# Kernel tuning notes

Measured on AMD Instinct MI355X. Metric: run time of the kernel, lower is better.

The kernel has to match this reference:

```python
import jax, jax.numpy as jnp
import numpy as np
from jax import lax

H = 2048          # hidden_size
NAH = 16          # num attn heads
AHD = H // NAH    # 128
NFH = 4           # num lact (fast-weight) heads
FHD = H // NFH    # 512 = d_in = d_out
DH = FHD          # d_h = d_in * inter_multi (1.0)
WIN = 1024        # sliding window
CHUNK = 512       # lact chunk size
B, S = 2, 2048
ROPE_BASE = 500000.0
EPS = 1e-6
BASE_LR_INV = 0.001 + float(np.log(-np.expm1(-0.001)))  # inv_softplus(1e-3)


def rms_norm(x, w):
    return x * lax.rsqrt(jnp.mean(x * x, axis=-1, keepdims=True) + EPS) * w


def silu(x):
    return x * jax.nn.sigmoid(x)


def silu_backprop(dy, x):
    sg = jax.nn.sigmoid(x)
    return dy * sg * (1.0 + x * (1.0 - sg))


def apply_rope(q, k):
    # q,k: [b,s,h,d]; non-interleaved (half-split) rotary, matching flash-attn RotaryEmbedding
    d = q.shape[-1]
    inv_freq = 1.0 / (ROPE_BASE ** (jnp.arange(0, d, 2, dtype=jnp.float32) / d))
    t = jnp.arange(q.shape[1], dtype=jnp.float32)
    freqs = jnp.outer(t, inv_freq)                       # [s, d/2]
    cos = jnp.cos(freqs)[None, :, None, :]
    sin = jnp.sin(freqs)[None, :, None, :]
    def rot(x):
        x1, x2 = jnp.split(x, 2, axis=-1)
        return jnp.concatenate([x1 * cos - x2 * sin, x2 * cos + x1 * sin], axis=-1)
    return rot(q), rot(k)


def sliding_window_attn(q, k, v):
    # [b,s,h,d]; causal sliding-window attention
    s = q.shape[1]
    scale = 1.0 / np.sqrt(q.shape[-1])
    i = jnp.arange(s)[:, None]
    j = jnp.arange(s)[None, :]
    mask = (j <= i) & (i - j < WIN)                      # [s,s]
    scores = jnp.einsum('bihd,bjhd->bhij', q, k) * scale
    scores = jnp.where(mask[None, None], scores, -jnp.inf)
    p = jax.nn.softmax(scores, axis=-1)
    return jnp.einsum('bhij,bjhd->bihd', p, v)


def setup_inputs() -> dict:
    key = jax.random.key(0)
    ks = jax.random.split(key, 10)
    def n(k, shape, scale):
        return jax.random.normal(k, shape, dtype=jnp.float32) * scale
    return {
        'hidden_states': n(ks[0], (B, S, H), 1.0),
        'attn_qkv_w': n(ks[1], (3 * H, H), 0.02),
        'attn_o_w': n(ks[2], (H, H), 0.02),
        'q_norm_w': jnp.ones((H,), jnp.float32),
        'k_norm_w': jnp.ones((H,), jnp.float32),
        'mlp_norm_w': jnp.ones((H,), jnp.float32),
        'mlp_qkv_w': n(ks[3], (3 * NFH * FHD, H), 0.02),
        'mlp_o_w': n(ks[4], (H, NFH * FHD), 0.02),
        'lr_w': n(ks[5], (3 * NFH, H), 0.02),
        'lr_b': jnp.zeros((3 * NFH,), jnp.float32),
        'w0': n(ks[6], (NFH, DH, FHD), 1.0 / np.sqrt(FHD)),
        'w1': n(ks[7], (NFH, FHD, DH), 1.0 / np.sqrt(DH)),
        'w2': n(ks[8], (NFH, DH, FHD), 1.0 / np.sqrt(FHD)),
        'ttt_norm_w': jnp.ones((FHD,), jnp.float32),
    }


def _forward(hidden_states, attn_qkv_w, attn_o_w, q_norm_w, k_norm_w, mlp_norm_w,
             mlp_qkv_w, mlp_o_w, lr_w, lr_b, w0, w1, w2, ttt_norm_w):
    b, s, _ = hidden_states.shape
    # ---- sliding window attention (token mixer) ----
    qkv = hidden_states @ attn_qkv_w.T
    q, k, v = jnp.split(qkv, 3, axis=-1)
    q = rms_norm(q, q_norm_w)
    k = rms_norm(k, k_norm_w)
    q = q.reshape(b, s, NAH, AHD)
    k = k.reshape(b, s, NAH, AHD)
    v = v.reshape(b, s, NAH, AHD)
    q, k = apply_rope(q, k)
    o = sliding_window_attn(q, k, v)
    attn_out = o.reshape(b, s, H) @ attn_o_w.T

    # ---- TTT-MLP SwiGLU fast-weight channel mixer after SWA ----
    x = rms_norm(attn_out, mlp_norm_w)
    fqkv = x @ mlp_qkv_w.T
    fq, fk, fv = jnp.split(fqkv, 3, axis=-1)
    fq, fk, fv = silu(fq), silu(fk), silu(fv)
    fq = fq.reshape(b, s, NFH, FHD)
    fk = fk.reshape(b, s, NFH, FHD)
    fv = fv.reshape(b, s, NFH, FHD)
    fq = fq / jnp.clip(jnp.linalg.norm(fq, axis=-1, keepdims=True), 1e-6)
    fk = fk / jnp.clip(jnp.linalg.norm(fk, axis=-1, keepdims=True), 1e-6)

    # per-token lrs (mamba parameterization: softplus(proj + inv_softplus(base_lr)))
    lr = jax.nn.softplus(x @ lr_w.T + lr_b + BASE_LR_INV)   # [b,s,3*NFH]
    l0, l1, l2 = jnp.split(lr, 3, axis=-1)                  # each [b,s,NFH]

    nc = s // CHUNK
    def chunkify(t):  # [b,s,h,d] -> [nc,b,h,c,d]
        return t.reshape(b, nc, CHUNK, t.shape[2], t.shape[3]).transpose(1, 0, 3, 2, 4)
    qs = chunkify(fq)
    ks_ = chunkify(fk)
    vs = chunkify(fv)
    l0s = chunkify(l0[..., None])
    l1s = chunkify(l1[..., None])
    l2s = chunkify(l2[..., None])

    w0b = jnp.broadcast_to(w0[None], (b,) + w0.shape)
    w1b = jnp.broadcast_to(w1[None], (b,) + w1.shape)
    w2b = jnp.broadcast_to(w2[None], (b,) + w2.shape)

    def step(carry, inp):
        cw0, cw1, cw2 = carry
        qc, kc, vc, lr0, lr1, lr2 = inp   # qc/kc/vc: [b,h,c,d]; lr*: [b,h,c,1]
        # apply current fast weights to queries of this chunk (apply-then-update)
        gq = jnp.einsum('bhed,bhcd->bhce', cw0, qc)
        hq = silu(gq) * jnp.einsum('bhed,bhcd->bhce', cw2, qc)
        oc = jnp.einsum('bhoe,bhce->bhco', cw1, hq)
        # update fast weights with this chunk's (k, v) under negative dot-product loss
        gk = jnp.einsum('bhed,bhcd->bhce', cw0, kc)      # gate pre-act
        hbm = jnp.einsum('bhed,bhcd->bhce', cw2, kc)     # hidden before mul
        hid = silu(gk) * hbm
        dhid = jnp.einsum('bhoe,bhco->bhce', cw1, vc)    # grad wrt hidden
        dhbm = dhid * silu(gk)
        dgate = dhid * hbm
        dgpre = silu_backprop(dgate, gk)
        nw1 = cw1 + jnp.einsum('bhco,bhce->bhoe', vc * lr1, hid)
        nw0 = cw0 + jnp.einsum('bhce,bhcd->bhed', dgpre, kc * lr0)
        nw2 = cw2 + jnp.einsum('bhce,bhcd->bhed', dhbm, kc * lr2)
        return (nw0, nw1, nw2), oc

    _, ocs = lax.scan(step, (w0b, w1b, w2b), (qs, ks_, vs, l0s, l1s, l2s))
    o_fw = ocs.transpose(1, 0, 3, 2, 4).reshape(b, s, NFH, FHD)
    o_fw = rms_norm(o_fw, ttt_norm_w)
    ttt_out = o_fw.reshape(b, s, NFH * FHD) @ mlp_o_w.T
    return attn_out + ttt_out


def reference(hidden_states, attn_qkv_w, attn_o_w, q_norm_w, k_norm_w, mlp_norm_w,
              mlp_qkv_w, mlp_o_w, lr_w, lr_b, w0, w1, w2, ttt_norm_w):
    return _forward(hidden_states, attn_qkv_w, attn_o_w, q_norm_w, k_norm_w, mlp_norm_w,
                    mlp_qkv_w, mlp_o_w, lr_w, lr_b, w0, w1, w2, ttt_norm_w)
```

## Files before the change

kernel.cpp:

```cpp
#include <hip/hip_runtime.h>
#include <cmath>

typedef unsigned short u16;
typedef unsigned int u32;
typedef short s16x8 __attribute__((ext_vector_type(8)));
typedef short s16x4 __attribute__((ext_vector_type(4)));
typedef float f32x4 __attribute__((ext_vector_type(4)));

#define DEV static __device__ __forceinline__

DEV float b2f(u16 h) { return __uint_as_float(((u32)h) << 16); }
DEV u16 f2b(float f) {
  u32 u = __float_as_uint(f);
  u = (u + 0x7FFFu + ((u >> 16) & 1u)) >> 16;
  return (u16)u;
}
DEV float siluf(float x) { return x / (1.f + __expf(-x)); }

DEV void gload16(const void* g, void* l) {
  __builtin_amdgcn_global_load_lds((const __attribute__((address_space(1))) void*)g,
                                   (__attribute__((address_space(3))) void*)l, 16, 0, 0);
}

struct GemmDesc {
  const u16* A; const u16* B;
  float* C; const float* Cin;
  u16* Cb; u16* CbT;
  long sAb, sAh, sBb, sBh, sCb_, sCh_, sCbb, sCbh, sCtb, sCth;
  int lda, ldb, ldc, ldcb, ldct, K;
};
struct GemmBatch { GemmDesc d[5]; int nbh; };

__global__ __launch_bounds__(256) void gemm_bt(GemmBatch gb) {
  int di = blockIdx.z / gb.nbh;
  int bh = blockIdx.z % gb.nbh;
  GemmDesc d = gb.d[di];
  __shared__ __align__(16) u16 As[2][4096];
  __shared__ __align__(16) u16 Bs[2][4096];
  int tid = threadIdx.x, w = tid >> 6, l = tid & 63;
  int b2 = bh >> 2, h2 = bh & 3;
  const u16* Ab = d.A + (long)b2 * d.sAb + (long)h2 * d.sAh + (long)blockIdx.y * 128 * d.lda;
  const u16* Bb = d.B + (long)b2 * d.sBb + (long)h2 * d.sBh + (long)blockIdx.x * 128 * d.ldb;
  int srow = l >> 2, scol = (l & 3) * 8;
  f32x4 acc[4][4] = {};
  int nk = d.K >> 5;

  auto stage = [&](int buf, int kt) {
    #pragma unroll
    for (int i = 0; i < 2; ++i) {
      int chunk = i * 4 + w;
      int row = chunk * 16 + srow;
      gload16(Ab + (long)row * d.lda + kt * 32 + scol, &As[buf][chunk * 512]);
      gload16(Bb + (long)row * d.ldb + kt * 32 + scol, &Bs[buf][chunk * 512]);
    }
  };

  stage(0, 0);
  asm volatile("s_waitcnt vmcnt(0)" ::: "memory");
  __syncthreads();

  int wr = (w >> 1) * 64, wc = (w & 1) * 64;
  int fro = l & 15, fko = (l >> 4) * 8;

  for (int kt = 0; kt < nk; ++kt) {
    int buf = kt & 1;
    if (kt + 1 < nk) stage(buf ^ 1, kt + 1);
    s16x8 af[4], bfr[4];
    #pragma unroll
    for (int m = 0; m < 4; ++m) af[m] = *(const s16x8*)&As[buf][(wr + m * 16 + fro) * 32 + fko];
    #pragma unroll
    for (int n = 0; n < 4; ++n) bfr[n] = *(const s16x8*)&Bs[buf][(wc + n * 16 + fro) * 32 + fko];
    #pragma unroll
    for (int m = 0; m < 4; ++m)
      #pragma unroll
      for (int n = 0; n < 4; ++n)
        acc[m][n] = __builtin_amdgcn_mfma_f32_16x16x32_bf16(af[m], bfr[n], acc[m][n], 0, 0, 0);
    asm volatile("s_waitcnt vmcnt(0)" ::: "memory");
    __syncthreads();
  }

  float* Cp = d.C ? d.C + (long)b2 * d.sCb_ + (long)h2 * d.sCh_ : nullptr;
  const float* Ci = d.Cin ? d.Cin + (long)b2 * d.sCb_ + (long)h2 * d.sCh_ : nullptr;
  u16* Cbp = d.Cb ? d.Cb + (long)b2 * d.sCbb + (long)h2 * d.sCbh : nullptr;
  u16* Ctp = d.CbT ? d.CbT + (long)b2 * d.sCtb + (long)h2 * d.sCth : nullptr;
  long rbase = (long)blockIdx.y * 128 + wr + (l >> 4) * 4;
  long cbase = (long)blockIdx.x * 128 + wc + (l & 15);
  #pragma unroll
  for (int m = 0; m < 4; ++m)
    #pragma unroll
    for (int n = 0; n < 4; ++n)
      #pragma unroll
      for (int j = 0; j < 4; ++j) {
        long r = rbase + m * 16 + j;
        long c = cbase + n * 16;
        float v = acc[m][n][j];
        if (Ci) v += Ci[r * d.ldc + c];
        if (Cp) Cp[r * d.ldc + c] = v;
        if (Cbp) Cbp[r * d.ldcb + c] = f2b(v);
        if (Ctp) Ctp[c * d.ldct + r] = f2b(v);
      }
}

__global__ __launch_bounds__(256) void convk(const float* __restrict__ in, u16* __restrict__ outp) {
  long i = ((long)blockIdx.x * 256 + threadIdx.x) * 4;
  float4 v = *(const float4*)(in + i);
  u16 o[4] __attribute__((aligned(8))) = {f2b(v.x), f2b(v.y), f2b(v.z), f2b(v.w)};
  *(s16x4*)&outp[i] = *(const s16x4*)o;
}

__global__ __launch_bounds__(256) void norm_rope_kernel(const u16* __restrict__ qkv,
    const float* __restrict__ qw, const float* __restrict__ kw,
    u16* __restrict__ qg, u16* __restrict__ kg, u16* __restrict__ vg) {
  __shared__ float qsh[2048], ksh[2048];
  __shared__ float red[2][4];
  int t = blockIdx.x, tid = threadIdx.x, w = tid >> 6, l = tid & 63;
  int s = t & 2047;
  const u16* row = qkv + (long)t * 6144;
  s16x8 vq = *(const s16x8*)&row[tid * 8];
  s16x8 vk = *(const s16x8*)&row[2048 + tid * 8];
  float sq = 0.f, sk = 0.f;
  #pragma unroll
  for (int i = 0; i < 8; ++i) {
    float a = b2f((u16)vq[i]); qsh[tid * 8 + i] = a; sq += a * a;
    float c = b2f((u16)vk[i]); ksh[tid * 8 + i] = c; sk += c * c;
  }
  *(s16x8*)&vg[(long)t * 2048 + tid * 8] = *(const s16x8*)&row[4096 + tid * 8];
  #pragma unroll
  for (int mk = 32; mk; mk >>= 1) { sq += __shfl_xor(sq, mk, 64); sk += __shfl_xor(sk, mk, 64); }
  if (l == 0) { red[0][w] = sq; red[1][w] = sk; }
  __syncthreads();
  float rq = rsqrtf((red[0][0] + red[0][1] + red[0][2] + red[0][3]) * (1.f / 2048.f) + 1e-6f);
  float rk = rsqrtf((red[1][0] + red[1][1] + red[1][2] + red[1][3]) * (1.f / 2048.f) + 1e-6f);
  const float lf = 13.122363377404329f / 64.f;
  #pragma unroll
  for (int ii = 0; ii < 4; ++ii) {
    int pid = tid + 256 * ii;
    int h = pid >> 6, dpos = pid & 63;
    float invf = expf(-(float)dpos * lf);
    float ang = (float)s * invf;
    float sn, cs;
    sincosf(ang, &sn, &cs);
    int i1 = h * 128 + dpos, i2 = i1 + 64;
    float q1 = qsh[i1] * rq * qw[i1], q2 = qsh[i2] * rq * qw[i2];
    qg[(long)t * 2048 + i1] = f2b(q1 * cs - q2 * sn);
    qg[(long)t * 2048 + i2] = f2b(q2 * cs + q1 * sn);
    float k1 = ksh[i1] * rk * kw[i1], k2v = ksh[i2] * rk * kw[i2];
    kg[(long)t * 2048 + i1] = f2b(k1 * cs - k2v * sn);
    kg[(long)t * 2048 + i2] = f2b(k2v * cs + k1 * sn);
  }
}

__global__ __launch_bounds__(256) void vtrans_kernel(const u16* __restrict__ v, u16* __restrict__ vT) {
  __shared__ u16 T[64][74];
  int tid = threadIdx.x;
  int bh = blockIdx.z, b = bh >> 4, h = bh & 15;
  int ts = blockIdx.x * 64, dg = blockIdx.y * 64;
  int r = tid >> 2, c0 = (tid & 3) * 16;
  const u16* src = v + ((long)b * 2048 + ts + r) * 2048 + h * 128 + dg + c0;
  *(s16x8*)&T[r][c0] = *(const s16x8*)src;
  *(s16x8*)&T[r][c0 + 8] = *(const s16x8*)(src + 8);
  __syncthreads();
  int d = tid >> 2, tg = (tid & 3) * 16;
  u16 a[16] __attribute__((aligned(16)));
  #pragma unroll
  for (int j = 0; j < 16; ++j) a[j] = T[tg + j][d];
  u16* dst = vT + ((long)bh * 128 + dg + d) * 2048 + ts + tg;
  *(s16x8*)dst = ((const s16x8*)a)[0];
  *(s16x8*)(dst + 8) = ((const s16x8*)a)[1];
}

__global__ __launch_bounds__(256, 3) void attn_kernel(const u16* __restrict__ qg, const u16* __restrict__ kg,
                                                      const u16* __restrict__ vT, u16* __restrict__ og) {
  __shared__ __align__(16) u16 Ks[64][136];
  __shared__ __align__(16) u16 Vt[128][72];
  __shared__ __align__(16) u16 Ps[4][16][72];
  int tid = threadIdx.x, w = tid >> 6, l = tid & 63;
  int h = blockIdx.y, b = blockIdx.z;
  int qs = blockIdx.x * 64;
  long tokb = (long)b * 2048;
  int fr = l & 15, fg = l >> 4;
  int wrow = qs + w * 16;

  s16x8 qf[4];
  #pragma unroll
  for (int ks = 0; ks < 4; ++ks)
    qf[ks] = *(const s16x8*)&qg[(tokb + wrow + fr) * 2048 + h * 128 + ks * 32 + fg * 8];

  f32x4 oacc[8] = {};
  float mrun[4], lrun[4];
  #pragma unroll
  for (int j = 0; j < 4; ++j) { mrun[j] = -__builtin_inff(); lrun[j] = 0.f; }

  int lo = qs - 1023;
  int t0 = lo > 0 ? (lo >> 6) : 0;
  int t1 = (qs + 63) >> 6;
  const float scale = 0.088388347648318447f;

  const u16* kbase = kg + tokb * 2048 + h * 128;
  const u16* vbase = vT + (long)(b * 16 + h) * 128 * 2048;

  s16x8 kreg[4], vreg[4];
  auto loadrg = [&](int kvs) {
    #pragma unroll
    for (int it = 0; it < 4; ++it) {
      int idx = it * 256 + tid;
      kreg[it] = *(const s16x8*)&kbase[(long)(kvs + (idx >> 4)) * 2048 + (idx & 15) * 8];
      vreg[it] = *(const s16x8*)&vbase[(long)(idx >> 3) * 2048 + kvs + (idx & 7) * 8];
    }
  };
  auto writelds = [&]() {
    #pragma unroll
    for (int it = 0; it < 4; ++it) {
      int idx = it * 256 + tid;
      *(s16x8*)&Ks[idx >> 4][(idx & 15) * 8] = kreg[it];
      *(s16x8*)&Vt[idx >> 3][(idx & 7) * 8] = vreg[it];
    }
  };

  loadrg(t0 << 6);
  writelds();
  __syncthreads();

  for (int kt = t0; kt <= t1; ++kt) {
    int kvs = kt << 6;
    if (kt < t1) loadrg((kt + 1) << 6);
    bool active = (kvs <= wrow + 15);
    if (active) {
      f32x4 st[4] = {};
      #pragma unroll
      for (int ct = 0; ct < 4; ++ct)
        #pragma unroll
        for (int ks = 0; ks < 4; ++ks) {
          s16x8 kf = *(const s16x8*)&Ks[ct * 16 + fr][ks * 32 + fg * 8];
          st[ct] = __builtin_amdgcn_mfma_f32_16x16x32_bf16(qf[ks], kf, st[ct], 0, 0, 0);
        }
      bool needm = (kvs + 63 > wrow) || (kvs < wrow - 1008);
      float mx[4];
      #pragma unroll
      for (int j = 0; j < 4; ++j) mx[j] = -__builtin_inff();
      #pragma unroll
      for (int ct = 0; ct < 4; ++ct)
        #pragma unroll
        for (int j = 0; j < 4; ++j) {
          float s = st[ct][j] * scale;
          if (needm) {
            int r = wrow + fg * 4 + j;
            int c = kvs + ct * 16 + fr;
            if (c > r || (r - c) >= 1024) s = -__builtin_inff();
          }
          st[ct][j] = s;
          mx[j] = fmaxf(mx[j], s);
        }
      #pragma unroll
      for (int mk = 8; mk; mk >>= 1)
        #pragma unroll
        for (int j = 0; j < 4; ++j) mx[j] = fmaxf(mx[j], __shfl_xor(mx[j], mk, 64));
      float sc[4], nmu[4], rs[4];
      #pragma unroll
      for (int j = 0; j < 4; ++j) {
        float nm = fmaxf(mrun[j], mx[j]);
        nmu[j] = (nm == -__builtin_inff()) ? 0.f : nm;
        sc[j] = __expf(mrun[j] - nmu[j]);
        mrun[j] = nm;
        rs[j] = 0.f;
      }
      #pragma unroll
      for (int ct = 0; ct < 4; ++ct)
        #pragma unroll
        for (int j = 0; j < 4; ++j) {
          float p = __expf(st[ct][j] - nmu[j]);
          rs[j] += p;
          Ps[w][fg * 4 + j][ct * 16 + fr] = f2b(p);
        }
      #pragma unroll
      for (int mk = 8; mk; mk >>= 1)
        #pragma unroll
        for (int j = 0; j < 4; ++j) rs[j] += __shfl_xor(rs[j], mk, 64);
      #pragma unroll
      for (int j = 0; j < 4; ++j) lrun[j] = lrun[j] * sc[j] + rs[j];
      #pragma unroll
      for (int dt = 0; dt < 8; ++dt)
        #pragma unroll
        for (int j = 0; j < 4; ++j) oacc[dt][j] *= sc[j];
      #pragma unroll
      for (int kst = 0; kst < 2; ++kst) {
        s16x8 pf = *(const s16x8*)&Ps[w][fr][kst * 32 + fg * 8];
        #pragma unroll
        for (int dt = 0; dt < 8; ++dt) {
          s16x8 vf = *(const s16x8*)&Vt[dt * 16 + fr][kst * 32 + fg * 8];
          oacc[dt] = __builtin_amdgcn_mfma_f32_16x16x32_bf16(pf, vf, oacc[dt], 0, 0, 0);
        }
      }
    }
    __syncthreads();
    if (kt < t1) {
      writelds();
    }
    __syncthreads();
  }
  #pragma unroll
  for (int j = 0; j < 4; ++j) {
    float inv = 1.f / lrun[j];
    long rofs = (tokb + wrow + fg * 4 + j) * 2048 + h * 128;
    #pragma unroll
    for (int dt = 0; dt < 8; ++dt)
      og[rofs + dt * 16 + fr] = f2b(oacc[dt][j] * inv);
  }
}

__global__ __launch_bounds__(256) void rms_x_kernel(const float* __restrict__ src, const float* __restrict__ wgt,
                                                    u16* __restrict__ dst) {
  __shared__ float red[4];
  int t = blockIdx.x, tid = threadIdx.x, w = tid >> 6, l = tid & 63;
  const float* row = src + (long)t * 2048;
  float v[8] __attribute__((aligned(16)));
  ((float4*)v)[0] = *(const float4*)&row[tid * 8];
  ((float4*)v)[1] = *(const float4*)&row[tid * 8 + 4];
  float ss = 0.f;
  #pragma unroll
  for (int i = 0; i < 8; ++i) ss += v[i] * v[i];
  #pragma unroll
  for (int mk = 32; mk; mk >>= 1) ss += __shfl_xor(ss, mk, 64);
  if (l == 0) red[w] = ss;
  __syncthreads();
  float r = rsqrtf((red[0] + red[1] + red[2] + red[3]) * (1.f / 2048.f) + 1e-6f);
  #pragma unroll
  for (int i = 0; i < 8; ++i) dst[(long)t * 2048 + tid * 8 + i] = f2b(v[i] * r * wgt[tid * 8 + i]);
}

__global__ __launch_bounds__(256) void lr_kernel(const u16* __restrict__ xb, const float* __restrict__ lrw,
                                                 const float* __restrict__ lrbias, float* __restrict__ lrout,
                                                 float base) {
  __shared__ float red[4][12];
  int t = blockIdx.x, tid = threadIdx.x, w = tid >> 6, l = tid & 63;
  float xv[8];
  s16x8 rv = *(const s16x8*)&xb[(long)t * 2048 + tid * 8];
  #pragma unroll
  for (int i = 0; i < 8; ++i) xv[i] = b2f((u16)rv[i]);
  float acc[12];
  #pragma unroll
  for (int j = 0; j < 12; ++j) {
    const float4* w4 = (const float4*)(lrw + j * 2048 + tid * 8);
    float4 a = w4[0], bq = w4[1];
    acc[j] = xv[0] * a.x + xv[1] * a.y + xv[2] * a.z + xv[3] * a.w +
             xv[4] * bq.x + xv[5] * bq.y + xv[6] * bq.z + xv[7] * bq.w;
  }
  #pragma unroll
  for (int j = 0; j < 12; ++j)
    #pragma unroll
    for (int mk = 32; mk; mk >>= 1) acc[j] += __shfl_xor(acc[j], mk, 64);
  if (l == 0) {
    #pragma unroll
    for (int j = 0; j < 12; ++j) red[w][j] = acc[j];
  }
  __syncthreads();
  if (tid < 12) {
    float s_ = red[0][tid] + red[1][tid] + red[2][tid] + red[3][tid] + lrbias[tid] + base;
    lrout[(long)t * 12 + tid] = (s_ > 20.f) ? s_ : log1pf(__expf(s_));
  }
}

__global__ __launch_bounds__(256) void silu_norm_kernel(const u16* __restrict__ fqkv,
    u16* __restrict__ fqo, u16* __restrict__ fko, u16* __restrict__ fvo) {
  int t = blockIdx.x, tid = threadIdx.x, w = tid >> 6, l = tid & 63;
  const u16* row = fqkv + (long)t * 6144;
  {
    s16x8 rv = *(const s16x8*)&row[w * 512 + l * 8];
    float x[8]; float ss = 0.f;
    #pragma unroll
    for (int i = 0; i < 8; ++i) { x[i] = siluf(b2f((u16)rv[i])); ss += x[i] * x[i]; }
    #pragma unroll
    for (int mk = 32; mk; mk >>= 1) ss += __shfl_xor(ss, mk, 64);
    float sc = 1.f / fmaxf(sqrtf(ss), 1e-6f);
    #pragma unroll
    for (int i = 0; i < 8; ++i) fqo[(long)t * 2048 + w * 512 + l * 8 + i] = f2b(x[i] * sc);
  }
  {
    s16x8 rv = *(const s16x8*)&row[2048 + w * 512 + l * 8];
    float x[8]; float ss = 0.f;
    #pragma unroll
    for (int i = 0; i < 8; ++i) { x[i] = siluf(b2f((u16)rv[i])); ss += x[i] * x[i]; }
    #pragma unroll
    for (int mk = 32; mk; mk >>= 1) ss += __shfl_xor(ss, mk, 64);
    float sc = 1.f / fmaxf(sqrtf(ss), 1e-6f);
    #pragma unroll
    for (int i = 0; i < 8; ++i) fko[(long)t * 2048 + w * 512 + l * 8 + i] = f2b(x[i] * sc);
  }
  {
    s16x8 rv = *(const s16x8*)&row[4096 + tid * 8];
    #pragma unroll
    for (int i = 0; i < 8; ++i) fvo[(long)t * 2048 + tid * 8 + i] = f2b(siluf(b2f((u16)rv[i])));
  }
}

__global__ __launch_bounds__(256) void winit_kernel(const float* __restrict__ w0, const float* __restrict__ w1,
                                                    const float* __restrict__ w2,
                                                    float* __restrict__ wbuf0, u16* __restrict__ wb16) {
  long gid = (long)blockIdx.x * 256 + threadIdx.x;
  long e4 = gid * 4;
  int which = (int)(e4 >> 21);
  long rem = e4 & 2097151L;
  int bh = (int)(rem >> 18);
  long idx = rem & 262143L;
  int h = bh & 3;
  const float* src = (which == 0 ? w0 : which == 1 ? w1 : w2) + (long)h * 262144 + idx;
  float4 v = *(const float4*)src;
  *(float4*)(wbuf0 + e4) = v;
  u16 o[4] __attribute__((aligned(8))) = {f2b(v.x), f2b(v.y), f2b(v.z), f2b(v.w)};
  *(s16x4*)&wb16[e4] = *(const s16x4*)o;
  if (which == 1) {
    u16* wt = wb16 + 3L * 2097152 + (long)bh * 262144;
    int r = (int)(idx >> 9), c = (int)(idx & 511);
    wt[(long)(c + 0) * 512 + r] = o[0];
    wt[(long)(c + 1) * 512 + r] = o[1];
    wt[(long)(c + 2) * 512 + r] = o[2];
    wt[(long)(c + 3) * 512 + r] = o[3];
  }
}

__global__ __launch_bounds__(256) void ttt_elem_kernel(
    const float* __restrict__ t5, u16* __restrict__ hqb,
    u16* __restrict__ hidT, u16* __restrict__ dhbmT, u16* __restrict__ dgpT,
    const u16* __restrict__ fk, const u16* __restrict__ fv, const float* __restrict__ lr,
    u16* __restrict__ k0T, u16* __restrict__ k2T, u16* __restrict__ v1T, int ic) {
  __shared__ u16 T0[64][72], T1[64][72], T2[64][72];
  int tid = threadIdx.x;
  int bh = blockIdx.y, b = bh >> 2, h = bh & 3;
  int tc = (blockIdx.x >> 3) * 64, te = (blockIdx.x & 7) * 64;
  int r = tid >> 2, c0 = (tid & 3) * 16;
  long base = (long)bh * 262144 + (long)(tc + r) * 512 + te + c0;

  {
    float gq_[16] __attribute__((aligned(16)));
    float q2_[16] __attribute__((aligned(16)));
    const float* pgq = t5 + base;
    const float* pq2 = t5 + 2097152L + base;
    #pragma unroll
    for (int q4 = 0; q4 < 4; ++q4) {
      ((float4*)gq_)[q4] = *(const float4*)(pgq + q4 * 4);
      ((float4*)q2_)[q4] = *(const float4*)(pq2 + q4 * 4);
    }
    u16 hq_[16] __attribute__((aligned(16)));
    #pragma unroll
    for (int i = 0; i < 16; ++i) hq_[i] = f2b(siluf(gq_[i]) * q2_[i]);
    *(s16x8*)&hqb[base] = ((const s16x8*)hq_)[0];
    *(s16x8*)&hqb[base + 8] = ((const s16x8*)hq_)[1];
  }
  {
    float gk_[16] __attribute__((aligned(16)));
    float k2_[16] __attribute__((aligned(16)));
    float dh_[16] __attribute__((aligned(16)));
    const float* pgk = t5 + 2L * 2097152 + base;
    const float* pk2 = t5 + 3L * 2097152 + base;
    const float* pdh = t5 + 4L * 2097152 + base;
    #pragma unroll
    for (int q4 = 0; q4 < 4; ++q4) {
      ((float4*)gk_)[q4] = *(const float4*)(pgk + q4 * 4);
      ((float4*)k2_)[q4] = *(const float4*)(pk2 + q4 * 4);
      ((float4*)dh_)[q4] = *(const float4*)(pdh + q4 * 4);
    }
    #pragma unroll
    for (int i = 0; i < 16; ++i) {
      float sg = 1.f / (1.f + __expf(-gk_[i]));
      float sil = gk_[i] * sg;
      float hid = sil * k2_[i];
      float dhbm = dh_[i] * sil;
      float dgate = dh_[i] * k2_[i];
      float dgp = dgate * sg * (1.f + gk_[i] * (1.f - sg));
      T0[r][c0 + i] = f2b(hid);
      T1[r][c0 + i] = f2b(dhbm);
      T2[r][c0 + i] = f2b(dgp);
    }
  }
  __syncthreads();
  long obase = (long)bh * 262144 + (long)(te + r) * 512 + tc + c0;
  {
    u16 a0[16] __attribute__((aligned(16))), a1[16] __attribute__((aligned(16))), a2[16] __attribute__((aligned(16)));
    #pragma unroll
    for (int i = 0; i < 16; ++i) { a0[i] = T0[c0 + i][r]; a1[i] = T1[c0 + i][r]; a2[i] = T2[c0 + i][r]; }
    *(s16x8*)&hidT[obase] = ((const s16x8*)a0)[0];   *(s16x8*)&hidT[obase + 8] = ((const s16x8*)a0)[1];
    *(s16x8*)&dhbmT[obase] = ((const s16x8*)a1)[0];  *(s16x8*)&dhbmT[obase + 8] = ((const s16x8*)a1)[1];
    *(s16x8*)&dgpT[obase] = ((const s16x8*)a2)[0];   *(s16x8*)&dgpT[obase + 8] = ((const s16x8*)a2)[1];
  }
  __syncthreads();
  {
    long to = (long)b * 2048 + (long)ic * 512 + tc + r;
    float l0 = lr[to * 12 + h], l1 = lr[to * 12 + 4 + h], l2 = lr[to * 12 + 8 + h];
    long goff = to * 2048 + (long)h * 512 + te + c0;
    s16x8 ka = *(const s16x8*)&fk[goff];
    s16x8 kb8 = *(const s16x8*)&fk[goff + 8];
    s16x8 va = *(const s16x8*)&fv[goff];
    s16x8 vb8 = *(const s16x8*)&fv[goff + 8];
    #pragma unroll
    for (int i = 0; i < 8; ++i) {
      float kv1 = b2f((u16)ka[i]), kv2 = b2f((u16)kb8[i]);
      float vv1 = b2f((u16)va[i]), vv2 = b2f((u16)vb8[i]);
      T0[r][c0 + i] = f2b(kv1 * l0);      T0[r][c0 + 8 + i] = f2b(kv2 * l0);
      T1[r][c0 + i] = f2b(kv1 * l2);      T1[r][c0 + 8 + i] = f2b(kv2 * l2);
      T2[r][c0 + i] = f2b(vv1 * l1);      T2[r][c0 + 8 + i] = f2b(vv2 * l1);
    }
  }
  __syncthreads();
  {
    u16 a0[16] __attribute__((aligned(16))), a1[16] __attribute__((aligned(16))), a2[16] __attribute__((aligned(16)));
    #pragma unroll
    for (int i = 0; i < 16; ++i) { a0[i] = T0[c0 + i][r]; a1[i] = T1[c0 + i][r]; a2[i] = T2[c0 + i][r]; }
    *(s16x8*)&k0T[obase] = ((const s16x8*)a0)[0];  *(s16x8*)&k0T[obase + 8] = ((const s16x8*)a0)[1];
    *(s16x8*)&k2T[obase] = ((const s16x8*)a1)[0];  *(s16x8*)&k2T[obase + 8] = ((const s16x8*)a1)[1];
    *(s16x8*)&v1T[obase] = ((const s16x8*)a2)[0];  *(s16x8*)&v1T[obase + 8] = ((const s16x8*)a2)[1];
  }
}

__global__ __launch_bounds__(256) void ttt_norm_kernel(const u16* __restrict__ src, const float* __restrict__ wgt,
                                                       u16* __restrict__ dst) {
  int t = blockIdx.x, tid = threadIdx.x, w = tid >> 6, l = tid & 63;
  long off = (long)t * 2048 + w * 512 + l * 8;
  s16x8 rv = *(const s16x8*)&src[off];
  float x[8];
  float ss = 0.f;
  #pragma unroll
  for (int i = 0; i < 8; ++i) { x[i] = b2f((u16)rv[i]); ss += x[i] * x[i]; }
  #pragma unroll
  for (int mk = 32; mk; mk >>= 1) ss += __shfl_xor(ss, mk, 64);
  float r = rsqrtf(ss * (1.f / 512.f) + 1e-6f);
  #pragma unroll
  for (int i = 0; i < 8; ++i) dst[off + i] = f2b(x[i] * r * wgt[l * 8 + i]);
}

extern "C" void kernel_launch(void* const* d_in, const int* in_sizes, int n_in,
                              void* d_out, int out_size, void* d_ws, size_t ws_size,
                              hipStream_t stream) {
  const float* hidden     = (const float*)d_in[0];
  const float* attn_qkv_w = (const float*)d_in[1];
  const float* attn_o_w   = (const float*)d_in[2];
  const float* q_norm_w   = (const float*)d_in[3];
  const float* k_norm_w   = (const float*)d_in[4];
  const float* mlp_norm_w = (const float*)d_in[5];
  const float* mlp_qkv_w  = (const float*)d_in[6];
  const float* mlp_o_w    = (const float*)d_in[7];
  const float* lr_w       = (const float*)d_in[8];
  const float* lr_bias    = (const float*)d_in[9];
  const float* w0in       = (const float*)d_in[10];
  const float* w1in       = (const float*)d_in[11];
  const float* w2in       = (const float*)d_in[12];
  const float* ttt_w      = (const float*)d_in[13];
  float* out = (float*)d_out;

  char* ws = (char*)d_ws;
  u16* hbf   = (u16*)(ws + 0);
  u16* wqb   = (u16*)(ws + 16777216);
  u16* wob   = (u16*)(ws + 41943040);
  char* big  = ws + 50331648;
  u16* qbuf  = (u16*)(ws + 121634816);
  u16* kbuf  = (u16*)(ws + 138412032);
  u16* vbuf  = (u16*)(ws + 155189248);
  u16* obuf  = (u16*)(ws + 171966464);
  float* lrb_ = (float*)(ws + 188743680);
  float* wbuf = (float*)(ws + 188940288);
  u16* wb16  = (u16*)(ws + 239271936);

  u16* qkvb = (u16*)big;
  u16* vTb  = (u16*)(big + 50331648);
  float* t5 = (float*)big;
  u16* hqb   = (u16*)(big + 41943040);
  u16* hidT  = (u16*)(big + 46137344);
  u16* dhbmT = (u16*)(big + 50331648);
  u16* dgpT  = (u16*)(big + 54525952);
  u16* k0T   = (u16*)(big + 58720256);
  u16* k2T   = (u16*)(big + 62914560);
  u16* v1T   = (u16*)(big + 67108864);
  u16* xb  = hbf;
  u16* ofw = hbf;

  convk<<<8192, 256, 0, stream>>>(hidden, hbf);
  convk<<<12288, 256, 0, stream>>>(attn_qkv_w, wqb);
  convk<<<4096, 256, 0, stream>>>(attn_o_w, wob);

  {
    GemmBatch g{}; g.nbh = 1;
    g.d[0].A = hbf; g.d[0].B = wqb; g.d[0].Cb = qkvb;
    g.d[0].lda = 2048; g.d[0].ldb = 2048; g.d[0].ldcb = 6144; g.d[0].K = 2048;
    gemm_bt<<<dim3(48, 32, 1), 256, 0, stream>>>(g);
  }
  norm_rope_kernel<<<4096, 256, 0, stream>>>(qkvb, q_norm_w, k_norm_w, qbuf, kbuf, vbuf);
  vtrans_kernel<<<dim3(32, 2, 32), 256, 0, stream>>>(vbuf, vTb);
  attn_kernel<<<dim3(32, 16, 2), 256, 0, stream>>>(qbuf, kbuf, vTb, obuf);
  {
    GemmBatch g{}; g.nbh = 1;
    g.d[0].A = obuf; g.d[0].B = wob; g.d[0].C = out;
    g.d[0].lda = 2048; g.d[0].ldb = 2048; g.d[0].ldc = 2048; g.d[0].K = 2048;
    gemm_bt<<<dim3(16, 32, 1), 256, 0, stream>>>(g);
  }
  rms_x_kernel<<<4096, 256, 0, stream>>>(out, mlp_norm_w, xb);
  convk<<<12288, 256, 0, stream>>>(mlp_qkv_w, wqb);
  convk<<<4096, 256, 0, stream>>>(mlp_o_w, wob);
  float base_lr_inv = 0.001f + logf(-expm1f(-0.001f));
  lr_kernel<<<4096, 256, 0, stream>>>(xb, lr_w, lr_bias, lrb_, base_lr_inv);
  {
    GemmBatch g{}; g.nbh = 1;
    g.d[0].A = xb; g.d[0].B = wqb; g.d[0].Cb = qkvb;
    g.d[0].lda = 2048; g.d[0].ldb = 2048; g.d[0].ldcb = 6144; g.d[0].K = 2048;
    gemm_bt<<<dim3(48, 32, 1), 256, 0, stream>>>(g);
  }
  silu_norm_kernel<<<4096, 256, 0, stream>>>(qkvb, qbuf, kbuf, vbuf);
  winit_kernel<<<6144, 256, 0, stream>>>(w0in, w1in, w2in, wbuf, wb16);

  for (int ic = 0; ic < 4; ++ic) {
    {
      GemmBatch g{}; g.nbh = 8;
      const u16* Asrc[5] = {qbuf, qbuf, kbuf, kbuf, vbuf};
      long Bwhich[5] = {0, 2, 0, 2, 3};
      for (int i = 0; i < 5; ++i) {
        GemmDesc& dd = g.d[i];
        dd.A = Asrc[i] + (long)ic * 1048576; dd.sAb = 4194304; dd.sAh = 512; dd.lda = 2048;
        dd.B = wb16 + Bwhich[i] * 2097152;   dd.sBb = 1048576; dd.sBh = 262144; dd.ldb = 512;
        dd.C = t5 + (long)i * 2097152;       dd.sCb_ = 1048576; dd.sCh_ = 262144; dd.ldc = 512;
        dd.K = 512;
      }
      gemm_bt<<<dim3(4, 4, 40), 256, 0, stream>>>(g);
    }
    ttt_elem_kernel<<<dim3(64, 8), 256, 0, stream>>>(t5, hqb, hidT, dhbmT, dgpT,
                                                     kbuf, vbuf, lrb_, k0T, k2T, v1T, ic);
    {
      GemmBatch g{}; g.nbh = 8;
      GemmDesc& dd = g.d[0];
      dd.A = hqb; dd.sAb = 1048576; dd.sAh = 262144; dd.lda = 512;
      dd.B = wb16 + 2097152; dd.sBb = 1048576; dd.sBh = 262144; dd.ldb = 512;
      dd.Cb = ofw + (long)ic * 1048576; dd.sCbb = 4194304; dd.sCbh = 512; dd.ldcb = 2048;
      dd.K = 512;
      gemm_bt<<<dim3(4, 4, 8), 256, 0, stream>>>(g);
    }
    {
      GemmBatch g{}; g.nbh = 8;
      float* wc_ = wbuf + (long)(ic & 1) * 6291456;
      float* wn_ = wbuf + (long)((ic & 1) ^ 1) * 6291456;
      const u16* A3[3] = {dgpT, v1T, dhbmT};
      const u16* B3[3] = {k0T, hidT, k2T};
      for (int i = 0; i < 3; ++i) {
        GemmDesc& dd = g.d[i];
        dd.A = A3[i]; dd.sAb = 1048576; dd.sAh = 262144; dd.lda = 512;
        dd.B = B3[i]; dd.sBb = 1048576; dd.sBh = 262144; dd.ldb = 512;
        dd.Cin = wc_ + (long)i * 2097152; dd.C = wn_ + (long)i * 2097152;
        dd.sCb_ = 1048576; dd.sCh_ = 262144; dd.ldc = 512;
        dd.Cb = wb16 + (long)i * 2097152; dd.sCbb = 1048576; dd.sCbh = 262144; dd.ldcb = 512;
        if (i == 1) { dd.CbT = wb16 + 3L * 2097152; dd.sCtb = 1048576; dd.sCth = 262144; dd.ldct = 512; }
        dd.K = 512;
      }
      gemm_bt<<<dim3(4, 4, 24), 256, 0, stream>>>(g);
    }
  }
  ttt_norm_kernel<<<4096, 256, 0, stream>>>(ofw, ttt_w, obuf);
  {
    GemmBatch g{}; g.nbh = 1;
    g.d[0].A = obuf; g.d[0].B = wob; g.d[0].C = out; g.d[0].Cin = out;
    g.d[0].lda = 2048; g.d[0].ldb = 2048; g.d[0].ldc = 2048; g.d[0].K = 2048;
    gemm_bt<<<dim3(16, 32, 1), 256, 0, stream>>>(g);
  }
  (void)in_sizes; (void)n_in; (void)out_size; (void)ws_size;
}
```

Baseline: 1.051 ms.

## Replace dense projection GEMMs with 256x256-tile pipelined MFMA kernel

Result: no change. 1.061 ms (+0.9%).

```diff
diff --git a/kernel.cpp b/kernel.cpp
--- a/kernel.cpp
+++ b/kernel.cpp
@@ -20,6 +20,107 @@
 DEV void gload16(const void* g, void* l) {
   __builtin_amdgcn_global_load_lds((const __attribute__((address_space(1))) void*)g,
                                    (__attribute__((address_space(3))) void*)l, 16, 0, 0);
+}
+
+DEV s16x8 lds_frag(const u16* buf, int row, int kg) {
+  int lin = row * 64 + kg * 16;
+  int adr = lin ^ (((row >> 1) & 3) << 4);
+  return *(const s16x8*)((const char*)buf + adr);
+}
+
+template <int MODE>
+__global__ __launch_bounds__(512, 2) void gemm256(const u16* __restrict__ A, const u16* __restrict__ B,
+                                                  void* __restrict__ Cout, const float* __restrict__ Cin,
+                                                  int ldc, int K, int gx) {
+  __shared__ __align__(16) u16 Al[4][256 * 32];
+  __shared__ __align__(16) u16 Bl[4][256 * 32];
+  int tid = threadIdx.x, w = tid >> 6, l = tid & 63;
+  int nwg = gridDim.x;
+  int wg = blockIdx.x;
+  int swzb = (wg & 7) * (nwg >> 3) + (wg >> 3);
+  int bx = swzb % gx, by = swzb / gx;
+  const u16* Ab = A + (long)by * 256 * K;
+  const u16* Bb = B + (long)bx * 256 * K;
+  int wr = w >> 2, wc = w & 3;
+  int fro = l & 15, kg = l >> 4;
+  f32x4 acc[8][4] = {};
+  int nk = K >> 5;
+
+  auto stageA = [&](int buf, int kt) {
+    #pragma unroll
+    for (int i = 0; i < 2; ++i) {
+      int x = (tid + i * 512) * 16;
+      int y = x ^ (((x >> 7) & 3) << 4);
+      gload16(Ab + (long)(y >> 6) * K + kt * 32 + ((y & 63) >> 1), (char*)&Al[buf][0] + x);
+    }
+  };
+  auto stageB = [&](int buf, int kt) {
+    #pragma unroll
+    for (int i = 0; i < 2; ++i) {
+      int x = (tid + i * 512) * 16;
+      int y = x ^ (((x >> 7) & 3) << 4);
+      gload16(Bb + (long)(y >> 6) * K + kt * 32 + ((y & 63) >> 1), (char*)&Bl[buf][0] + x);
+    }
+  };
+
+  stageA(0, 0); stageB(0, 0);
+  stageA(1, 1); stageB(1, 1);
+  stageA(2, 2); stageB(2, 2);
+  asm volatile("s_waitcnt vmcnt(8)" ::: "memory");
+  __builtin_amdgcn_s_barrier();
+
+  for (int t = 0; t < nk; ++t) {
+    int cur = t & 3;
+    const u16* Ac = &Al[cur][0];
+    const u16* Bc = &Bl[cur][0];
+    s16x8 af[8], bfr[4];
+    #pragma unroll
+    for (int m = 0; m < 4; ++m) af[m] = lds_frag(Ac, wr * 128 + m * 16 + fro, kg);
+    #pragma unroll
+    for (int n = 0; n < 4; ++n) bfr[n] = lds_frag(Bc, wc * 64 + n * 16 + fro, kg);
+    if (t + 3 < nk) stageA((t + 3) & 3, t + 3);
+    __builtin_amdgcn_s_barrier();
+    __builtin_amdgcn_s_setprio(1);
+    #pragma unroll
+    for (int m = 0; m < 4; ++m)
+      #pragma unroll
+      for (int n = 0; n < 4; ++n)
+        acc[m][n] = __builtin_amdgcn_mfma_f32_16x16x32_bf16(af[m], bfr[n], acc[m][n], 0, 0, 0);
+    __builtin_amdgcn_s_setprio(0);
+    __builtin_amdgcn_s_barrier();
+    #pragma unroll
+    for (int m = 0; m < 4; ++m) af[4 + m] = lds_frag(Ac, wr * 128 + (4 + m) * 16 + fro, kg);
+    if (t + 3 < nk) stageB((t + 3) & 3, t + 3);
+    __builtin_amdgcn_s_barrier();
+    __builtin_amdgcn_s_setprio(1);
+    #pragma unroll
+    for (int m = 0; m < 4; ++m)
+      #pragma unroll
+      for (int n = 0; n < 4; ++n)
+        acc[4 + m][n] = __builtin_amdgcn_mfma_f32_16x16x32_bf16(af[4 + m], bfr[n], acc[4 + m][n], 0, 0, 0);
+    __builtin_amdgcn_s_setprio(0);
+    int rem = nk - 1 - t;
+    if (rem > 2)       asm volatile("s_waitcnt vmcnt(8)" ::: "memory");
+    else if (rem == 2) asm volatile("s_waitcnt vmcnt(4)" ::: "memory");
+    else if (rem == 1) asm volatile("s_waitcnt vmcnt(0)" ::: "memory");
+    __builtin_amdgcn_s_barrier();
+  }
+
+  long rbase = (long)by * 256 + wr * 128 + kg * 4;
+  long cbase = (long)bx * 256 + wc * 64 + fro;
+  #pragma unroll
+  for (int m = 0; m < 8; ++m)
+    #pragma unroll
+    for (int n = 0; n < 4; ++n)
+      #pragma unroll
+      for (int j = 0; j < 4; ++j) {
+        long r = rbase + m * 16 + j;
+        long c = cbase + n * 16;
+        float v = acc[m][n][j];
+        if (MODE == 2) v += Cin[r * ldc + c];
+        if (MODE == 0) ((u16*)Cout)[r * ldc + c] = f2b(v);
+        else ((float*)Cout)[r * ldc + c] = v;
+      }
 }
 
 struct GemmDesc {
@@ -576,32 +677,17 @@
   convk<<<12288, 256, 0, stream>>>(attn_qkv_w, wqb);
   convk<<<4096, 256, 0, stream>>>(attn_o_w, wob);
 
-  {
-    GemmBatch g{}; g.nbh = 1;
-    g.d[0].A = hbf; g.d[0].B = wqb; g.d[0].Cb = qkvb;
-    g.d[0].lda = 2048; g.d[0].ldb = 2048; g.d[0].ldcb = 6144; g.d[0].K = 2048;
-    gemm_bt<<<dim3(48, 32, 1), 256, 0, stream>>>(g);
-  }
+  gemm256<0><<<384, 512, 0, stream>>>(hbf, wqb, qkvb, nullptr, 6144, 2048, 24);
   norm_rope_kernel<<<4096, 256, 0, stream>>>(qkvb, q_norm_w, k_norm_w, qbuf, kbuf, vbuf);
   vtrans_kernel<<<dim3(32, 2, 32), 256, 0, stream>>>(vbuf, vTb);
   attn_kernel<<<dim3(32, 16, 2), 256, 0, stream>>>(qbuf, kbuf, vTb, obuf);
-  {
-    GemmBatch g{}; g.nbh = 1;
-    g.d[0].A = obuf; g.d[0].B = wob; g.d[0].C = out;
-    g.d[0].lda = 2048; g.d[0].ldb = 2048; g.d[0].ldc = 2048; g.d[0].K = 2048;
-    gemm_bt<<<dim3(16, 32, 1), 256, 0, stream>>>(g);
-  }
+  gemm256<1><<<128, 512, 0, stream>>>(obuf, wob, out, nullptr, 2048, 2048, 8);
   rms_x_kernel<<<4096, 256, 0, stream>>>(out, mlp_norm_w, xb);
   convk<<<12288, 256, 0, stream>>>(mlp_qkv_w, wqb);
   convk<<<4096, 256, 0, stream>>>(mlp_o_w, wob);
   float base_lr_inv = 0.001f + logf(-expm1f(-0.001f));
   lr_kernel<<<4096, 256, 0, stream>>>(xb, lr_w, lr_bias, lrb_, base_lr_inv);
-  {
-    GemmBatch g{}; g.nbh = 1;
-    g.d[0].A = xb; g.d[0].B = wqb; g.d[0].Cb = qkvb;
-    g.d[0].lda = 2048; g.d[0].ldb = 2048; g.d[0].ldcb = 6144; g.d[0].K = 2048;
-    gemm_bt<<<dim3(48, 32, 1), 256, 0, stream>>>(g);
-  }
+  gemm256<0><<<384, 512, 0, stream>>>(xb, wqb, qkvb, nullptr, 6144, 2048, 24);
   silu_norm_kernel<<<4096, 256, 0, stream>>>(qkvb, qbuf, kbuf, vbuf);
   winit_kernel<<<6144, 256, 0, stream>>>(w0in, w1in, w2in, wbuf, wb16);
 
@@ -650,11 +736,6 @@
     }
   }
   ttt_norm_kernel<<<4096, 256, 0, stream>>>(ofw, ttt_w, obuf);
-  {
-    GemmBatch g{}; g.nbh = 1;
-    g.d[0].A = obuf; g.d[0].B = wob; g.d[0].C = out; g.d[0].Cin = out;
-    g.d[0].lda = 2048; g.d[0].ldb = 2048; g.d[0].ldc = 2048; g.d[0].K = 2048;
-    gemm_bt<<<dim3(16, 32, 1), 256, 0, stream>>>(g);
-  }
+  gemm256<2><<<128, 512, 0, stream>>>(obuf, wob, out, out, 2048, 2048, 8);
   (void)in_sizes; (void)n_in; (void)out_size; (void)ws_size;
 }
```
